# Optimization experiments

Hardware: AMD Instinct MI355X
Metric: run time of the kernel (lower is better)

The kernel has to match this reference:

```python
import jax, jax.numpy as jnp
import numpy as np

N = 2048
D = 128
E = 16384
NEG = -9e15


def setup_inputs() -> dict:
    key = jax.random.key(0)
    k1, k2, k3, k4, k5 = jax.random.split(key, 5)
    X_n = jax.random.normal(k1, (N, D), dtype=jnp.float32)
    edge_indices = jax.random.randint(k2, (2, E), 0, N, dtype=jnp.int64)
    adj = jax.random.randint(k3, (N, N), 0, 2, dtype=jnp.int32)
    W1 = jax.random.normal(k4, (D, D), dtype=jnp.float32) * (2.0 / D) ** 0.5
    W2 = jax.random.normal(k5, (1, 2 * D), dtype=jnp.float32) * (1.0 / D) ** 0.5
    return {"X_n": X_n, "edge_indices": edge_indices, "adj": adj, "W1": W1, "W2": W2}


def reference(X_n, edge_indices, adj, W1, W2):
    # f_w1: identity-activation Linear without bias -> X_n @ W1.T  [N, D]
    Xw = X_n @ W1.T
    d = Xw.shape[1]
    # f_w2 on concat(Xw[i], Xw[j]) decomposes into two rank-1 score vectors:
    # weight[i, j] = Xw[i] . W2[0, :d] + Xw[j] . W2[0, d:]
    s_i = Xw @ W2[0, :d]   # [N]
    s_j = Xw @ W2[0, d:]   # [N]
    weight = s_i[:, None] + s_j[None, :]            # [N, N]
    masked = jnp.where(adj > 0, weight, jnp.float32(NEG))
    attention = jax.nn.softmax(masked, axis=1)       # [N, N]
    src, dst = edge_indices[0], edge_indices[1]
    a_p = attention[dst, src]                        # [E]
    a_c = attention[src, dst]                        # [E]
    e = edge_indices.shape[1]
    cols = jnp.arange(e)
    atten_matrix = jnp.zeros((X_n.shape[0], 2 * e), dtype=jnp.float32)
    atten_matrix = atten_matrix.at[dst, cols].set(a_p)
    atten_matrix = atten_matrix.at[src, cols + e].set(a_c)
    return atten_matrix
```

## Files before the change

### kernel.cpp

```cpp
#include <hip/hip_runtime.h>

#define NN 2048
#define DD 128
#define EE 16384

__global__ void k_sj(const float* __restrict__ X, const float* __restrict__ W1,
                     const float* __restrict__ W2, float* __restrict__ ev) {
    __shared__ float u[DD];
    const int t = threadIdx.x;
    if (t < DD) {
        float acc = 0.f;
#pragma unroll 8
        for (int k = 0; k < DD; ++k) acc += W2[DD + k] * W1[k * DD + t];
        u[t] = acc;
    }
    __syncthreads();
    const int wave = t >> 6, lane = t & 63;
    const int row0 = blockIdx.x * 16 + wave * 4;
#pragma unroll
    for (int rr = 0; rr < 4; ++rr) {
        const int row = row0 + rr;
        const float2 v = ((const float2*)(X + (size_t)row * DD))[lane];
        float acc = v.x * u[2 * lane] + v.y * u[2 * lane + 1];
#pragma unroll
        for (int off = 32; off; off >>= 1) acc += __shfl_down(acc, off);
        if (lane == 0) ev[row] = expf(acc);
    }
}

__global__ void k_rowz(const int* __restrict__ adj, const float* __restrict__ ev,
                       float* __restrict__ Zv) {
    const int i = blockIdx.x;
    const int t = threadIdx.x;
    const int4* arow = (const int4*)(adj + (size_t)i * NN);
    const float4* ef = (const float4*)ev;
    float acc = 0.f;
#pragma unroll
    for (int b = 0; b < NN / 4; b += 256) {
        const int4   a  = arow[b + t];
        const float4 e4 = ef[b + t];
        acc += (float)a.x * e4.x + (float)a.y * e4.y +
               (float)a.z * e4.z + (float)a.w * e4.w;
    }
#pragma unroll
    for (int off = 32; off; off >>= 1) acc += __shfl_down(acc, off);
    __shared__ float wsum[4];
    if ((t & 63) == 0) wsum[t >> 6] = acc;
    __syncthreads();
    if (t == 0) Zv[i] = wsum[0] + wsum[1] + wsum[2] + wsum[3];
}

__global__ void k_edge(const int* __restrict__ ei, const int* __restrict__ adj,
                       const float* __restrict__ ev, const float* __restrict__ Zv,
                       float* __restrict__ out) {
    const int e = blockIdx.x * blockDim.x + threadIdx.x;
    if (e >= EE) return;
    const int s = ei[e];
    const int d = ei[EE + e];
    const float invn = 1.0f / (float)NN;

    const float zd = Zv[d];
    float ap;
    if (zd == 0.f) ap = invn;
    else ap = (adj[(size_t)d * NN + s] > 0) ? ev[s] / zd : 0.f;
    out[(size_t)d * (2 * EE) + e] = ap;

    const float zs = Zv[s];
    float ac;
    if (zs == 0.f) ac = invn;
    else ac = (adj[(size_t)s * NN + d] > 0) ? ev[d] / zs : 0.f;
    out[(size_t)s * (2 * EE) + EE + e] = ac;
}

extern "C" void kernel_launch(void* const* d_in, const int* in_sizes, int n_in,
                              void* d_out, int out_size, void* d_ws, size_t ws_size,
                              hipStream_t stream) {
    const float* X   = (const float*)d_in[0];
    const int*   ei  = (const int*)d_in[1];
    const int*   adj = (const int*)d_in[2];
    const float* W1  = (const float*)d_in[3];
    const float* W2  = (const float*)d_in[4];
    float* out = (float*)d_out;

    float* ev = (float*)d_ws;
    float* Zv = ev + NN;

    hipMemsetAsync(d_out, 0, (size_t)out_size * sizeof(float), stream);

    k_sj  <<<NN / 16, 256, 0, stream>>>(X, W1, W2, ev);
    k_rowz<<<NN,      256, 0, stream>>>(adj, ev, Zv);
    k_edge<<<EE / 256, 256, 0, stream>>>(ei, adj, ev, Zv, out);
}
```

Baseline: 299.5 us.

## Replace memset plus scattered writes with a single dense output-writing pass

The edge kernel now stores each column's row index and value in workspace arrays instead of scattering into the output. A new dense kernel writes the whole 2048x32768 output once with vectorized nontemporal stores, choosing the value or zero per column. This drops the separate memset and the scattered stores. In exchange, every output element reads the compact column arrays again, and the workspace must hold the extra arrays.

New measurement: 292.5 us. -2.3%, faster.

```diff
diff --git a/kernel.cpp b/kernel.cpp
--- a/kernel.cpp
+++ b/kernel.cpp
@@ -3,6 +3,9 @@
 #define NN 2048
 #define DD 128
 #define EE 16384
+
+typedef float v4f __attribute__((ext_vector_type(4)));
+typedef int   v4i __attribute__((ext_vector_type(4)));
 
 __global__ void k_sj(const float* __restrict__ X, const float* __restrict__ W1,
                      const float* __restrict__ W2, float* __restrict__ ev) {
@@ -50,9 +53,9 @@
     if (t == 0) Zv[i] = wsum[0] + wsum[1] + wsum[2] + wsum[3];
 }
 
-__global__ void k_edge(const int* __restrict__ ei, const int* __restrict__ adj,
+__global__ void k_vals(const int* __restrict__ ei, const int* __restrict__ adj,
                        const float* __restrict__ ev, const float* __restrict__ Zv,
-                       float* __restrict__ out) {
+                       int* __restrict__ rowid, float* __restrict__ val) {
     const int e = blockIdx.x * blockDim.x + threadIdx.x;
     if (e >= EE) return;
     const int s = ei[e];
@@ -63,13 +66,30 @@
     float ap;
     if (zd == 0.f) ap = invn;
     else ap = (adj[(size_t)d * NN + s] > 0) ? ev[s] / zd : 0.f;
-    out[(size_t)d * (2 * EE) + e] = ap;
 
     const float zs = Zv[s];
     float ac;
     if (zs == 0.f) ac = invn;
     else ac = (adj[(size_t)s * NN + d] > 0) ? ev[d] / zs : 0.f;
-    out[(size_t)s * (2 * EE) + EE + e] = ac;
+
+    rowid[e]      = d;  val[e]      = ap;
+    rowid[EE + e] = s;  val[EE + e] = ac;
+}
+
+__global__ __launch_bounds__(256) void k_write(const int* __restrict__ rowid,
+                                               const float* __restrict__ val,
+                                               v4f* __restrict__ out4) {
+    const int l  = blockIdx.x * 256 + threadIdx.x;
+    const int r  = l >> 13;
+    const int c4 = l & 8191;
+    const v4i rid = ((const v4i*)rowid)[c4];
+    const v4f vv  = ((const v4f*)val)[c4];
+    v4f o;
+    o.x = (rid.x == r) ? vv.x : 0.f;
+    o.y = (rid.y == r) ? vv.y : 0.f;
+    o.z = (rid.z == r) ? vv.z : 0.f;
+    o.w = (rid.w == r) ? vv.w : 0.f;
+    __builtin_nontemporal_store(o, out4 + l);
 }
 
 extern "C" void kernel_launch(void* const* d_in, const int* in_sizes, int n_in,
@@ -80,14 +100,16 @@
     const int*   adj = (const int*)d_in[2];
     const float* W1  = (const float*)d_in[3];
     const float* W2  = (const float*)d_in[4];
-    float* out = (float*)d_out;
 
-    float* ev = (float*)d_ws;
-    float* Zv = ev + NN;
+    float* ev    = (float*)d_ws;
+    float* Zv    = ev + NN;
+    float* val   = Zv + NN;
+    int*   rowid = (int*)(val + 2 * EE);
 
-    hipMemsetAsync(d_out, 0, (size_t)out_size * sizeof(float), stream);
+    k_sj   <<<NN / 16,  256, 0, stream>>>(X, W1, W2, ev);
+    k_rowz <<<NN,       256, 0, stream>>>(adj, ev, Zv);
+    k_vals <<<EE / 256, 256, 0, stream>>>(ei, adj, ev, Zv, rowid, val);
 
-    k_sj  <<<NN / 16, 256, 0, stream>>>(X, W1, W2, ev);
-    k_rowz<<<NN,      256, 0, stream>>>(adj, ev, Zv);
-    k_edge<<<EE / 256, 256, 0, stream>>>(ei, adj, ev, Zv, out);
+    const int n4 = out_size / 4;
+    k_write<<<n4 / 256, 256, 0, stream>>>(rowid, val, (v4f*)d_out);
 }
```
